# Performance work log

Hardware: AMD Instinct MI355X
Metric: run time of the kernel (lower is better)

## Reference

```python
import jax, jax.numpy as jnp
import numpy as np

EPS = 1e-12  # matches torch.nn.functional.normalize eps

def _l2norm(x, axis=-1):
    n = jnp.sqrt(jnp.sum(x * x, axis=axis, keepdims=True))
    return x / jnp.maximum(n, EPS)

def setup_inputs() -> dict:
    key = jax.random.key(0)
    k1, k2 = jax.random.split(key)
    B, C, H, W = 16, 256, 32, 32
    K = 8192
    z = jax.random.normal(k1, (B, C, H, W), dtype=jnp.float32)
    # torch init: uniform(-1/K, 1/K)
    emb_weight = jax.random.uniform(k2, (K, C), dtype=jnp.float32,
                                    minval=-1.0 / K, maxval=1.0 / K)
    return {"z": z, "emb_weight": emb_weight}

def reference(z, emb_weight):
    B, C, H, W = z.shape
    zt = jnp.transpose(z, (0, 2, 3, 1))            # [B,H,W,C]
    z_flat = zt.reshape(-1, C)                      # [N,C]
    zf_n = _l2norm(z_flat)                          # normalized tokens
    e_n = _l2norm(emb_weight)                       # normalized codebook [K,C]
    # squared euclidean distance via matmul (N x K)
    d = (jnp.sum(zf_n * zf_n, axis=1, keepdims=True)
         + jnp.sum(e_n * e_n, axis=1)
         - 2.0 * jnp.einsum('nc,kc->nk', zf_n, e_n))
    idx = jnp.argmin(d, axis=1)                     # [N]
    # get_codebook_entry: gather raw weight then normalize
    zq = _l2norm(emb_weight[idx])                   # [N,C]
    zq = zq.reshape(B, H, W, C)
    z_n = _l2norm(zt)                               # normalize z over channel dim
    # straight-through estimator
    zq = z_n + jax.lax.stop_gradient(zq - z_n)
    out = jnp.transpose(zq, (0, 3, 1, 2))           # [B,C,H,W]
    indices = idx.reshape(B, H, W)
    return out, indices
```

## Files before the change

### kernel.cpp

```cpp
#include <hip/hip_runtime.h>
#include <math.h>
#include <float.h>

#define K_CODES 8192
#define C_DIM   256
#define N_TOK   16384
#define B_      16
#define H_      32
#define W_      32
#define HW      1024
#define KSPLIT  16
#define TOKS_PER_BLK 256

typedef short  short8   __attribute__((ext_vector_type(8)));
typedef float  floatx16 __attribute__((ext_vector_type(16)));

__device__ inline ushort f32_to_bf16_rne(float x) {
    union { float f; unsigned u; } v; v.f = x;
    unsigned u = v.u;
    return (ushort)((u + 0x7FFFu + ((u >> 16) & 1u)) >> 16);
}
__device__ inline float bf16_bits_to_f32(ushort h) {
    union { unsigned u; float f; } v; v.u = ((unsigned)h) << 16;
    return v.f;
}
__device__ inline unsigned umax_(unsigned a, unsigned b) { return a > b ? a : b; }
__device__ inline unsigned umin_(unsigned a, unsigned b) { return a < b ? a : b; }

__device__ inline void g2l16(const void* g, void* l) {
    __builtin_amdgcn_global_load_lds((const __attribute__((address_space(1))) unsigned int*)g,
                                     (__attribute__((address_space(3))) unsigned int*)l,
                                     16, 0, 0);
}


__global__ __launch_bounds__(256) void norm_pack(
        const float* __restrict__ emb, const float* __restrict__ z,
        float* __restrict__ e_n, float* __restrict__ s2,
        ushort* __restrict__ Chi,
        float* __restrict__ ztn, ushort* __restrict__ Thi) {
    __shared__ float tile[32][257];
    __shared__ float pvt[32][9];
    __shared__ float pvt2[32][9];
    __shared__ float inv[32];
    int t = threadIdx.x;
    int bid = blockIdx.x;
    if (bid < 256) {
        int k0 = bid * 32;
        int r = t >> 3, cp = t & 7;
        const float* src = emb + (size_t)(k0 + r) * C_DIM + cp * 32;
        float ss = 0.f;
        #pragma unroll
        for (int j = 0; j < 8; ++j) {
            float4 v = *(const float4*)(src + j * 4);
            tile[r][cp * 32 + j * 4 + 0] = v.x;
            tile[r][cp * 32 + j * 4 + 1] = v.y;
            tile[r][cp * 32 + j * 4 + 2] = v.z;
            tile[r][cp * 32 + j * 4 + 3] = v.w;
            ss = fmaf(v.x, v.x, ss); ss = fmaf(v.y, v.y, ss);
            ss = fmaf(v.z, v.z, ss); ss = fmaf(v.w, v.w, ss);
        }
        pvt[r][cp] = ss;
        __syncthreads();
        if (t < 32) {
            float a = 0.f;
            #pragma unroll
            for (int p = 0; p < 8; ++p) a += pvt[t][p];
            inv[t] = 1.0f / fmaxf(sqrtf(a), 1e-12f);
        }
        __syncthreads();
        float iv = inv[r];
        float s2p = 0.f;
        float* dst = e_n + (size_t)(k0 + r) * C_DIM + cp * 32;
        #pragma unroll
        for (int j = 0; j < 8; ++j) {
            float a = tile[r][cp * 32 + j * 4 + 0] * iv;
            float b = tile[r][cp * 32 + j * 4 + 1] * iv;
            float c = tile[r][cp * 32 + j * 4 + 2] * iv;
            float d = tile[r][cp * 32 + j * 4 + 3] * iv;
            s2p = fmaf(a, a, s2p); s2p = fmaf(b, b, s2p);
            s2p = fmaf(c, c, s2p); s2p = fmaf(d, d, s2p);
            float4 o = {a, b, c, d};
            *(float4*)(dst + j * 4) = o;
        }
        pvt2[r][cp] = s2p;
        __syncthreads();
        if (t < 32) {
            float a = 0.f;
            #pragma unroll
            for (int p = 0; p < 8; ++p) a += pvt2[t][p];
            s2[k0 + t] = a;
        }
        char* chiB = (char*)Chi;
        #pragma unroll
        for (int e = 0; e < 4; ++e) {
            int p = e * 256 + t;
            int row = p & 31;
            int ch0 = ((p >> 6) << 4) | (((p >> 5) & 1) << 3);
            float rv = inv[row];
            union { ushort u[8]; uint4 v; } hs;
            #pragma unroll
            for (int i = 0; i < 8; ++i)
                hs.u[i] = f32_to_bf16_rne(tile[row][ch0 + i] * rv);
            size_t addr = (size_t)bid * 16384 + (size_t)p * 16;
            *(uint4*)(chiB + addr) = hs.v;
        }
    } else {
        int tb = bid - 256;
        int b = tb >> 5, h = tb & 31;
        const float* zb = z + ((size_t)(b * C_DIM) * H_ + h) * W_;
        int c0 = t >> 3, wq = t & 7;
        #pragma unroll
        for (int it = 0; it < 8; ++it) {
            int c = it * 32 + c0;
            float4 v = *(const float4*)(zb + (size_t)c * HW + wq * 4);
            tile[wq * 4 + 0][c] = v.x;
            tile[wq * 4 + 1][c] = v.y;
            tile[wq * 4 + 2][c] = v.z;
            tile[wq * 4 + 3][c] = v.w;
        }
        __syncthreads();
        int part = t >> 5, w2 = t & 31;
        float s = 0.f;
        #pragma unroll
        for (int i = 0; i < 32; ++i) {
            float v = tile[w2][part * 32 + i];
            s = fmaf(v, v, s);
        }
        pvt[w2][part] = s;
        __syncthreads();
        if (t < 32) {
            float ss = 0.f;
            #pragma unroll
            for (int p = 0; p < 8; ++p) ss += pvt[t][p];
            inv[t] = 1.0f / fmaxf(sqrtf(ss), 1e-12f);
        }
        __syncthreads();
        int n_base = tb * 32;
        for (int r = 0; r < 32; ++r) {
            float val = tile[r][t] * inv[r];
            ztn[(size_t)(n_base + r) * C_DIM + t] = val;
        }
        char* thiB = (char*)Thi;
        #pragma unroll
        for (int e = 0; e < 4; ++e) {
            int p = e * 256 + t;
            int row = p & 31;
            int ch0 = ((p >> 6) << 4) | (((p >> 5) & 1) << 3);
            float rv = inv[row];
            union { ushort u[8]; uint4 v; } hs;
            #pragma unroll
            for (int i = 0; i < 8; ++i)
                hs.u[i] = f32_to_bf16_rne(tile[row][ch0 + i] * rv);
            size_t addr = (size_t)tb * 16384 + (size_t)p * 16;
            *(uint4*)(thiB + addr) = hs.v;
        }
    }
}

__global__ __launch_bounds__(256, 2) void score_topk(
        const ushort* __restrict__ Chi,
        const ushort* __restrict__ Thi, uint2* __restrict__ cand) {
    __shared__ __align__(16) char smem[24576];
    int t = threadIdx.x;
    int l = t & 63, wv = t >> 6;
    int hh = l >> 5, col = l & 31;
    int tokBase = blockIdx.x * TOKS_PER_BLK;
    int tokRG = tokBase >> 5;
    int part = blockIdx.y;
    int partBase = part * (K_CODES / KSPLIT);
    int codeRGbase = partBase >> 5;

    const char* chiB = (const char*)Chi;
    const char* thiB = (const char*)Thi;

    unsigned rv1[2] = {0u, 0u}, rv2[2] = {0u, 0u}, rv3[2] = {0u, 0u};
    int ri1[2] = {0, 0}, ri2[2] = {0, 0}, ri3[2] = {0, 0};

    auto stage = [&](int skt, int ss, char* buf) {
        int codeRG = codeRGbase + skt * 4;
        #pragma unroll
        for (int gi = 0; gi < 3; ++gi) {
            int slice = wv * 3 + gi;
            const char* gb;
            int off;
            if (slice < 4) {
                gb = chiB + (size_t)(codeRG + slice) * 16384;
                off = slice << 10;
            } else {
                int trg = slice - 4;
                gb = thiB + (size_t)(tokRG + trg) * 16384;
                off = 4096 + (trg << 10);
            }
            g2l16(gb + ss * 1024 + (l << 4), buf + off);
        }
    };

    stage(0, 0, smem);

    for (int kt = 0; kt < 4; ++kt) {
        floatx16 acc[4][2];
        #pragma unroll
        for (int ct = 0; ct < 4; ++ct)
            #pragma unroll
            for (int nt = 0; nt < 2; ++nt)
                #pragma unroll
                for (int r = 0; r < 16; ++r) acc[ct][nt][r] = 0.f;

        for (int s = 0; s < 16; ++s) {
            int gidx = kt * 16 + s;
            __syncthreads();
            int nidx = gidx + 1;
            if (nidx < 64)
                stage(nidx >> 4, nidx & 15, smem + ((nidx & 1) ? 12288 : 0));
            const char* buf = smem + ((gidx & 1) ? 12288 : 0);

            short8 bh[2];
            #pragma unroll
            for (int nt = 0; nt < 2; ++nt) {
                int trg = wv * 2 + nt;
                bh[nt] = *(const short8*)(buf + 4096 + (trg << 10) + (l << 4));
            }
            #pragma unroll
            for (int ct = 0; ct < 4; ++ct) {
                short8 ah = *(const short8*)(buf + (ct << 10) + (l << 4));
                #pragma unroll
                for (int nt = 0; nt < 2; ++nt) {
                    acc[ct][nt] = __builtin_amdgcn_mfma_f32_32x32x16_bf16(ah, bh[nt], acc[ct][nt], 0, 0, 0);
                }
            }
        }

        int kbase = partBase + kt * 128;
        #pragma unroll
        for (int nt = 0; nt < 2; ++nt) {
            unsigned m1 = 0u, m2 = 0u, m3 = 0u;
            #pragma unroll
            for (int ct = 0; ct < 4; ++ct) {
                #pragma unroll
                for (int r = 0; r < 16; ++r) {
                    unsigned key = (__float_as_uint(fmaf(acc[ct][nt][r], 0.25f, 1.25f)) & 0xFFFFFFC0u)
                                   | (unsigned)((ct << 4) | r);
                    unsigned t1 = umin_(m1, key); m1 = umax_(m1, key);
                    unsigned t2 = umin_(m2, t1);  m2 = umax_(m2, t1);
                    m3 = umax_(m3, t2);
                }
            }
            unsigned mm[3] = {m1, m2, m3};
            #pragma unroll
            for (int j = 0; j < 3; ++j) {
                unsigned k = mm[j];
                int o = (int)(k & 63u), r = o & 15;
                int c = kbase + ((o >> 4) << 5) + (r & 3) + 8 * (r >> 2) + 4 * hh;
                if (k > rv1[nt]) {
                    rv3[nt] = rv2[nt]; ri3[nt] = ri2[nt];
                    rv2[nt] = rv1[nt]; ri2[nt] = ri1[nt];
                    rv1[nt] = k; ri1[nt] = c;
                } else if (k > rv2[nt]) {
                    rv3[nt] = rv2[nt]; ri3[nt] = ri2[nt];
                    rv2[nt] = k; ri2[nt] = c;
                } else if (k > rv3[nt]) {
                    rv3[nt] = k; ri3[nt] = c;
                }
            }
        }
    }

    __syncthreads();
    unsigned* mk = (unsigned*)smem;
    int*      mi = (int*)(smem + 8192);
    #pragma unroll
    for (int nt = 0; nt < 2; ++nt) {
        int base = (wv * 64 + nt * 32 + col) * 6 + hh * 3;
        mk[base + 0] = rv1[nt]; mi[base + 0] = ri1[nt];
        mk[base + 1] = rv2[nt]; mi[base + 1] = ri2[nt];
        mk[base + 2] = rv3[nt]; mi[base + 2] = ri3[nt];
    }
    __syncthreads();
    {
        unsigned b1 = 0u, b2 = 0u, b3 = 0u;
        int i1 = 0x7FFFFFFF, i2 = 0x7FFFFFFF, i3 = 0x7FFFFFFF;
        #pragma unroll
        for (int j = 0; j < 6; ++j) {
            unsigned k = mk[t * 6 + j]; int i = mi[t * 6 + j];
            if (k > b1 || (k == b1 && i < i1)) {
                b3 = b2; i3 = i2; b2 = b1; i2 = i1; b1 = k; i1 = i;
            } else if (k > b2 || (k == b2 && i < i2)) {
                b3 = b2; i3 = i2; b2 = k; i2 = i;
            } else if (k > b3 || (k == b3 && i < i3)) {
                b3 = k; i3 = i;
            }
        }
        size_t base = ((size_t)part * N_TOK + tokBase + t) * 3;
        cand[base + 0] = {b1, (unsigned)i1};
        cand[base + 1] = {b2, (unsigned)i2};
        cand[base + 2] = {b3, (unsigned)i3};
    }
}

__global__ __launch_bounds__(256) void rescore_gather(
        const float* __restrict__ ztn, const float* __restrict__ e_n,
        const float* __restrict__ s2, const uint2* __restrict__ cand,
        float* __restrict__ out, float* __restrict__ idxf) {
    __shared__ __align__(16) char sm[32 * 257 * 4];
    __shared__ uint2 cd[32][48];
    __shared__ int idxs[32];
    __shared__ int slowlist[32];
    __shared__ unsigned bkey[32];
    __shared__ int nslow;
    float* tile = (float*)sm;
    int t = threadIdx.x;
    int bid = blockIdx.x;
    int b = bid >> 5, h = bid & 31;
    int n_base = bid * 32;
    int wv = t >> 6, l = t & 63;

    if (t == 0) nslow = 0;
    {
        int tok = t >> 3, p = t & 7;
        int n = n_base + tok;
        #pragma unroll
        for (int slot = 0; slot < 3; ++slot) {
            cd[tok][p * 3 + slot]        = cand[((size_t)p * N_TOK + n) * 3 + slot];
            cd[tok][(p + 8) * 3 + slot]  = cand[((size_t)(p + 8) * N_TOK + n) * 3 + slot];
        }
    }
    __syncthreads();

    if (t < 32) {
        unsigned b1k = 0u, b2k = 0u; int b1i = 0x7FFFFFFF, b2i = 0x7FFFFFFF;
        #pragma unroll
        for (int p = 0; p < 48; ++p) {
            uint2 c2 = cd[t][p];
            unsigned k = c2.x; int i = (int)c2.y;
            if (k > b1k || (k == b1k && i < b1i)) { b2k = b1k; b2i = b1i; b1k = k; b1i = i; }
            else if (k > b2k || (k == b2k && i < b2i)) { b2k = k; b2i = i; }
        }
        bkey[t] = b1k;
        if (b1k - b2k > 2048u) {
            idxs[t] = b1i;
            idxf[n_base + t] = (float)b1i;
        } else {
            int s = atomicAdd(&nslow, 1);
            slowlist[s] = t;
        }
    }
    __syncthreads();
    int ns = nslow;
    for (int j = wv; j < ns; j += 4) {
        int tok = slowlist[j];
        int n = n_base + tok;
        unsigned bk = bkey[tok];
        float bs = FLT_MAX; int bi = 0x7FFFFFFF;
        if (l < 48) {
            uint2 c2 = cd[tok][l];
            if (c2.x + 8192u >= bk) {
                int c = (int)c2.y;
                const float* er = e_n + (size_t)c * C_DIM;
                const float* zr = ztn + (size_t)n * C_DIM;
                float s = 0.f;
                #pragma unroll
                for (int jj = 0; jj < 64; ++jj) {
                    float4 e4 = *(const float4*)(er + jj * 4);
                    float4 z4 = *(const float4*)(zr + jj * 4);
                    s = fmaf(e4.x, z4.x, s); s = fmaf(e4.y, z4.y, s);
                    s = fmaf(e4.z, z4.z, s); s = fmaf(e4.w, z4.w, s);
                }
                bs = s2[c] - 2.f * s;
                bi = c;
            }
        }
        #pragma unroll
        for (int d = 1; d < 64; d <<= 1) {
            float os = __shfl_xor(bs, d);
            int   oi = __shfl_xor(bi, d);
            if (os < bs || (os == bs && oi < bi)) { bs = os; bi = oi; }
        }
        if (l == 0) { idxs[tok] = bi; idxf[n] = (float)bi; }
    }
    __syncthreads();

    for (int r = 0; r < 32; ++r) {
        int k = idxs[r];
        tile[r * 257 + t] = e_n[(size_t)k * C_DIM + t];
    }
    __syncthreads();
    int w = t & 31, c0 = t >> 5;
    float* ob = out + ((size_t)(b * C_DIM) * H_ + h) * W_;
    #pragma unroll
    for (int it = 0; it < 32; ++it) {
        int c = it * 8 + c0;
        ob[(size_t)c * HW + w] = tile[w * 257 + c];
    }
}

extern "C" void kernel_launch(void* const* d_in, const int* in_sizes, int n_in,
                              void* d_out, int out_size, void* d_ws, size_t ws_size,
                              hipStream_t stream) {
    const float* z   = (const float*)d_in[0];
    const float* emb = (const float*)d_in[1];
    float* out  = (float*)d_out;
    float* idxf = out + (size_t)B_ * C_DIM * H_ * W_;

    char* ws = (char*)d_ws;
    size_t o = 0;
    float*  e_n  = (float*)(ws + o);  o += (size_t)K_CODES * C_DIM * 4;
    float*  s2   = (float*)(ws + o);  o += 32768;
    float*  ztn  = (float*)(ws + o);  o += (size_t)N_TOK * C_DIM * 4;
    ushort* Chi  = (ushort*)(ws + o); o += (size_t)K_CODES * C_DIM * 2;
    ushort* Thi  = (ushort*)(ws + o); o += (size_t)N_TOK * C_DIM * 2;
    uint2*  cand = (uint2*)(ws + o);  o += (size_t)KSPLIT * N_TOK * 3 * 8;

    hipLaunchKernelGGL(norm_pack, dim3(256 + B_ * H_), dim3(256), 0, stream,
                       emb, z, e_n, s2, Chi, ztn, Thi);
    hipLaunchKernelGGL(score_topk, dim3(N_TOK / TOKS_PER_BLK, KSPLIT), dim3(256), 0, stream,
                       Chi, Thi, cand);
    hipLaunchKernelGGL(rescore_gather, dim3(B_ * H_), dim3(256), 0, stream,
                       ztn, e_n, s2, cand, out, idxf);
}
```

Baseline: 176.5 us.

## Split score tile into 2x2 wave grid with 128-token blocks and higher occupancy

The score_topk block tile shrinks from 256 tokens to 128 tokens per block, and the four waves are arranged as a 2x2 grid over codes and tokens instead of each wave covering all codes. The kernel now uses 16KB of LDS and launch bounds allow 4 blocks per CU, aiming for better latency hiding and more blocks to spread across CUs. Staging uses precomputed global pointers advanced per step, and the final merge reduces 12 candidates per token instead of 6. In exchange each block reuses less data, since the codebook slice is streamed once per 128 tokens rather than per 256, which doubles codebook traffic.

Measured after the change: 208.4 us. 18.0% more time.

```diff
diff --git a/kernel.cpp b/kernel.cpp
--- a/kernel.cpp
+++ b/kernel.cpp
@@ -10,7 +10,7 @@
 #define W_      32
 #define HW      1024
 #define KSPLIT  16
-#define TOKS_PER_BLK 256
+#define TOKS_PER_BLK 128
 
 typedef short  short8   __attribute__((ext_vector_type(8)));
 typedef float  floatx16 __attribute__((ext_vector_type(16)));
@@ -158,13 +158,14 @@
     }
 }
 
-__global__ __launch_bounds__(256, 2) void score_topk(
+__global__ __launch_bounds__(256, 4) void score_topk(
         const ushort* __restrict__ Chi,
         const ushort* __restrict__ Thi, uint2* __restrict__ cand) {
-    __shared__ __align__(16) char smem[24576];
+    __shared__ __align__(16) char smem[16384];
     int t = threadIdx.x;
     int l = t & 63, wv = t >> 6;
     int hh = l >> 5, col = l & 31;
+    int wr = wv >> 1, wc = wv & 1;
     int tokBase = blockIdx.x * TOKS_PER_BLK;
     int tokRG = tokBase >> 5;
     int part = blockIdx.y;
@@ -174,61 +175,62 @@
     const char* chiB = (const char*)Chi;
     const char* thiB = (const char*)Thi;
 
+    const char* gp[2];
+    int ldo[2];
+    int dkt[2];
+    #pragma unroll
+    for (int gi = 0; gi < 2; ++gi) {
+        int sl = wv * 2 + gi;
+        if (sl < 4) {
+            gp[gi]  = chiB + (size_t)(codeRGbase + sl) * 16384 + (l << 4);
+            ldo[gi] = sl << 10;
+            dkt[gi] = 4 * 16384 - 15 * 1024;
+        } else {
+            int trg = sl - 4;
+            gp[gi]  = thiB + (size_t)(tokRG + trg) * 16384 + (l << 4);
+            ldo[gi] = 4096 + (trg << 10);
+            dkt[gi] = -15 * 1024;
+        }
+    }
+    auto issue = [&](int parity) {
+        char* base = smem + (parity ? 8192 : 0);
+        g2l16(gp[0], base + ldo[0]);
+        g2l16(gp[1], base + ldo[1]);
+    };
+    auto advance = [&](int snum) {
+        bool kb = (snum & 15) == 15;
+        gp[0] += kb ? dkt[0] : 1024;
+        gp[1] += kb ? dkt[1] : 1024;
+    };
+
+    issue(0); advance(0);
+
     unsigned rv1[2] = {0u, 0u}, rv2[2] = {0u, 0u}, rv3[2] = {0u, 0u};
     int ri1[2] = {0, 0}, ri2[2] = {0, 0}, ri3[2] = {0, 0};
 
-    auto stage = [&](int skt, int ss, char* buf) {
-        int codeRG = codeRGbase + skt * 4;
-        #pragma unroll
-        for (int gi = 0; gi < 3; ++gi) {
-            int slice = wv * 3 + gi;
-            const char* gb;
-            int off;
-            if (slice < 4) {
-                gb = chiB + (size_t)(codeRG + slice) * 16384;
-                off = slice << 10;
-            } else {
-                int trg = slice - 4;
-                gb = thiB + (size_t)(tokRG + trg) * 16384;
-                off = 4096 + (trg << 10);
-            }
-            g2l16(gb + ss * 1024 + (l << 4), buf + off);
-        }
-    };
-
-    stage(0, 0, smem);
-
     for (int kt = 0; kt < 4; ++kt) {
-        floatx16 acc[4][2];
-        #pragma unroll
-        for (int ct = 0; ct < 4; ++ct)
+        floatx16 acc[2][2];
+        #pragma unroll
+        for (int ct = 0; ct < 2; ++ct)
             #pragma unroll
             for (int nt = 0; nt < 2; ++nt)
                 #pragma unroll
                 for (int r = 0; r < 16; ++r) acc[ct][nt][r] = 0.f;
 
-        for (int s = 0; s < 16; ++s) {
-            int gidx = kt * 16 + s;
+        for (int ss = 0; ss < 16; ++ss) {
+            int g = kt * 16 + ss;
             __syncthreads();
-            int nidx = gidx + 1;
-            if (nidx < 64)
-                stage(nidx >> 4, nidx & 15, smem + ((nidx & 1) ? 12288 : 0));
-            const char* buf = smem + ((gidx & 1) ? 12288 : 0);
-
-            short8 bh[2];
-            #pragma unroll
-            for (int nt = 0; nt < 2; ++nt) {
-                int trg = wv * 2 + nt;
-                bh[nt] = *(const short8*)(buf + 4096 + (trg << 10) + (l << 4));
-            }
-            #pragma unroll
-            for (int ct = 0; ct < 4; ++ct) {
-                short8 ah = *(const short8*)(buf + (ct << 10) + (l << 4));
-                #pragma unroll
-                for (int nt = 0; nt < 2; ++nt) {
-                    acc[ct][nt] = __builtin_amdgcn_mfma_f32_32x32x16_bf16(ah, bh[nt], acc[ct][nt], 0, 0, 0);
-                }
-            }
+            if (g + 1 < 64) { issue((g + 1) & 1); advance(g + 1); }
+            const char* buf = smem + ((g & 1) ? 8192 : 0);
+
+            short8 ah0 = *(const short8*)(buf + (((wc << 1) | 0) << 10) + (l << 4));
+            short8 ah1 = *(const short8*)(buf + (((wc << 1) | 1) << 10) + (l << 4));
+            short8 bh0 = *(const short8*)(buf + 4096 + (((wr << 1) | 0) << 10) + (l << 4));
+            short8 bh1 = *(const short8*)(buf + 4096 + (((wr << 1) | 1) << 10) + (l << 4));
+            acc[0][0] = __builtin_amdgcn_mfma_f32_32x32x16_bf16(ah0, bh0, acc[0][0], 0, 0, 0);
+            acc[0][1] = __builtin_amdgcn_mfma_f32_32x32x16_bf16(ah0, bh1, acc[0][1], 0, 0, 0);
+            acc[1][0] = __builtin_amdgcn_mfma_f32_32x32x16_bf16(ah1, bh0, acc[1][0], 0, 0, 0);
+            acc[1][1] = __builtin_amdgcn_mfma_f32_32x32x16_bf16(ah1, bh1, acc[1][1], 0, 0, 0);
         }
 
         int kbase = partBase + kt * 128;
@@ -236,11 +238,11 @@
         for (int nt = 0; nt < 2; ++nt) {
             unsigned m1 = 0u, m2 = 0u, m3 = 0u;
             #pragma unroll
-            for (int ct = 0; ct < 4; ++ct) {
+            for (int ct = 0; ct < 2; ++ct) {
                 #pragma unroll
                 for (int r = 0; r < 16; ++r) {
                     unsigned key = (__float_as_uint(fmaf(acc[ct][nt][r], 0.25f, 1.25f)) & 0xFFFFFFC0u)
-                                   | (unsigned)((ct << 4) | r);
+                                   | (unsigned)(((((wc << 1) | ct)) << 4) | r);
                     unsigned t1 = umin_(m1, key); m1 = umax_(m1, key);
                     unsigned t2 = umin_(m2, t1);  m2 = umax_(m2, t1);
                     m3 = umax_(m3, t2);
@@ -271,18 +273,18 @@
     int*      mi = (int*)(smem + 8192);
     #pragma unroll
     for (int nt = 0; nt < 2; ++nt) {
-        int base = (wv * 64 + nt * 32 + col) * 6 + hh * 3;
+        int base = (wr * 64 + nt * 32 + col) * 12 + (((wc << 1) | hh)) * 3;
         mk[base + 0] = rv1[nt]; mi[base + 0] = ri1[nt];
         mk[base + 1] = rv2[nt]; mi[base + 1] = ri2[nt];
         mk[base + 2] = rv3[nt]; mi[base + 2] = ri3[nt];
     }
     __syncthreads();
-    {
+    if (t < 128) {
         unsigned b1 = 0u, b2 = 0u, b3 = 0u;
         int i1 = 0x7FFFFFFF, i2 = 0x7FFFFFFF, i3 = 0x7FFFFFFF;
         #pragma unroll
-        for (int j = 0; j < 6; ++j) {
-            unsigned k = mk[t * 6 + j]; int i = mi[t * 6 + j];
+        for (int j = 0; j < 12; ++j) {
+            unsigned k = mk[t * 12 + j]; int i = mi[t * 12 + j];
             if (k > b1 || (k == b1 && i < i1)) {
                 b3 = b2; i3 = i2; b2 = b1; i2 = i1; b1 = k; i1 = i;
             } else if (k > b2 || (k == b2 && i < i2)) {
```

## Split rescore and gather into separate decide_rescore and gather_out kernels

Applied to the files above, without the earlier changes.

Splits the combined rescore-and-gather kernel into two kernels. The first processes 256 tokens per block with one thread per token: it merges the candidates, writes the index directly, and rescores ambiguous tokens with one wavefront each, reading candidates straight from global memory. The second reads the indices back and does the transposed gather into the output. This is meant to parallelise the candidate merge across all threads, which previously ran on only 32 threads per block, and to balance the slow-path work. The cost is an extra launch and a round trip of the indices through memory.

Result: slower. 203.4 us (+15.2%).

```diff
diff --git a/kernel.cpp b/kernel.cpp
--- a/kernel.cpp
+++ b/kernel.cpp
@@ -19,10 +19,6 @@
     union { float f; unsigned u; } v; v.f = x;
     unsigned u = v.u;
     return (ushort)((u + 0x7FFFu + ((u >> 16) & 1u)) >> 16);
-}
-__device__ inline float bf16_bits_to_f32(ushort h) {
-    union { unsigned u; float f; } v; v.u = ((unsigned)h) << 16;
-    return v.f;
 }
 __device__ inline unsigned umax_(unsigned a, unsigned b) { return a > b ? a : b; }
 __device__ inline unsigned umin_(unsigned a, unsigned b) { return a < b ? a : b; }
@@ -298,90 +294,83 @@
     }
 }
 
-__global__ __launch_bounds__(256) void rescore_gather(
+__global__ __launch_bounds__(256) void decide_rescore(
         const float* __restrict__ ztn, const float* __restrict__ e_n,
         const float* __restrict__ s2, const uint2* __restrict__ cand,
-        float* __restrict__ out, float* __restrict__ idxf) {
-    __shared__ __align__(16) char sm[32 * 257 * 4];
-    __shared__ uint2 cd[32][48];
-    __shared__ int idxs[32];
-    __shared__ int slowlist[32];
-    __shared__ unsigned bkey[32];
+        float* __restrict__ idxf) {
+    __shared__ int slowlist[256];
+    __shared__ unsigned slowbk[256];
     __shared__ int nslow;
-    float* tile = (float*)sm;
+    int t = threadIdx.x;
+    int n0 = blockIdx.x * 256;
+    int wv = t >> 6, l = t & 63;
+    if (t == 0) nslow = 0;
+    __syncthreads();
+    {
+        int n = n0 + t;
+        unsigned b1k = 0u, b2k = 0u; int b1i = 0x7FFFFFFF, b2i = 0x7FFFFFFF;
+        for (int p = 0; p < 16; ++p) {
+            #pragma unroll
+            for (int s = 0; s < 3; ++s) {
+                uint2 c2 = cand[((size_t)p * N_TOK + n) * 3 + s];
+                unsigned k = c2.x; int i = (int)c2.y;
+                if (k > b1k || (k == b1k && i < b1i)) { b2k = b1k; b2i = b1i; b1k = k; b1i = i; }
+                else if (k > b2k || (k == b2k && i < b2i)) { b2k = k; b2i = i; }
+            }
+        }
+        if (b1k - b2k > 2048u) {
+            idxf[n] = (float)b1i;
+        } else {
+            int s = atomicAdd(&nslow, 1);
+            slowlist[s] = t; slowbk[s] = b1k;
+        }
+    }
+    __syncthreads();
+    int ns = nslow;
+    for (int j = wv; j < ns; j += 4) {
+        int tok = slowlist[j];
+        int n = n0 + tok;
+        unsigned bk = slowbk[j];
+        float bs = FLT_MAX; int bi = 0x7FFFFFFF;
+        if (l < 48) {
+            int p = l / 3, s = l - p * 3;
+            uint2 c2 = cand[((size_t)p * N_TOK + n) * 3 + s];
+            if (c2.x + 8192u >= bk) {
+                int c = (int)c2.y;
+                const float* er = e_n + (size_t)c * C_DIM;
+                const float* zr = ztn + (size_t)n * C_DIM;
+                float sdot = 0.f;
+                #pragma unroll
+                for (int jj = 0; jj < 64; ++jj) {
+                    float4 e4 = *(const float4*)(er + jj * 4);
+                    float4 z4 = *(const float4*)(zr + jj * 4);
+                    sdot = fmaf(e4.x, z4.x, sdot); sdot = fmaf(e4.y, z4.y, sdot);
+                    sdot = fmaf(e4.z, z4.z, sdot); sdot = fmaf(e4.w, z4.w, sdot);
+                }
+                bs = s2[c] - 2.f * sdot;
+                bi = c;
+            }
+        }
+        #pragma unroll
+        for (int d = 1; d < 64; d <<= 1) {
+            float os = __shfl_xor(bs, d);
+            int   oi = __shfl_xor(bi, d);
+            if (os < bs || (os == bs && oi < bi)) { bs = os; bi = oi; }
+        }
+        if (l == 0) idxf[n] = (float)bi;
+    }
+}
+
+__global__ __launch_bounds__(256) void gather_out(
+        const float* __restrict__ e_n, const float* __restrict__ idxf,
+        float* __restrict__ out) {
+    __shared__ float tile[32 * 257];
     int t = threadIdx.x;
     int bid = blockIdx.x;
     int b = bid >> 5, h = bid & 31;
     int n_base = bid * 32;
-    int wv = t >> 6, l = t & 63;
-
-    if (t == 0) nslow = 0;
-    {
-        int tok = t >> 3, p = t & 7;
-        int n = n_base + tok;
-        #pragma unroll
-        for (int slot = 0; slot < 3; ++slot) {
-            cd[tok][p * 3 + slot]        = cand[((size_t)p * N_TOK + n) * 3 + slot];
-            cd[tok][(p + 8) * 3 + slot]  = cand[((size_t)(p + 8) * N_TOK + n) * 3 + slot];
-        }
-    }
-    __syncthreads();
-
-    if (t < 32) {
-        unsigned b1k = 0u, b2k = 0u; int b1i = 0x7FFFFFFF, b2i = 0x7FFFFFFF;
-        #pragma unroll
-        for (int p = 0; p < 48; ++p) {
-            uint2 c2 = cd[t][p];
-            unsigned k = c2.x; int i = (int)c2.y;
-            if (k > b1k || (k == b1k && i < b1i)) { b2k = b1k; b2i = b1i; b1k = k; b1i = i; }
-            else if (k > b2k || (k == b2k && i < b2i)) { b2k = k; b2i = i; }
-        }
-        bkey[t] = b1k;
-        if (b1k - b2k > 2048u) {
-            idxs[t] = b1i;
-            idxf[n_base + t] = (float)b1i;
-        } else {
-            int s = atomicAdd(&nslow, 1);
-            slowlist[s] = t;
-        }
-    }
-    __syncthreads();
-    int ns = nslow;
-    for (int j = wv; j < ns; j += 4) {
-        int tok = slowlist[j];
-        int n = n_base + tok;
-        unsigned bk = bkey[tok];
-        float bs = FLT_MAX; int bi = 0x7FFFFFFF;
-        if (l < 48) {
-            uint2 c2 = cd[tok][l];
-            if (c2.x + 8192u >= bk) {
-                int c = (int)c2.y;
-                const float* er = e_n + (size_t)c * C_DIM;
-                const float* zr = ztn + (size_t)n * C_DIM;
-                float s = 0.f;
-                #pragma unroll
-                for (int jj = 0; jj < 64; ++jj) {
-                    float4 e4 = *(const float4*)(er + jj * 4);
-                    float4 z4 = *(const float4*)(zr + jj * 4);
-                    s = fmaf(e4.x, z4.x, s); s = fmaf(e4.y, z4.y, s);
-                    s = fmaf(e4.z, z4.z, s); s = fmaf(e4.w, z4.w, s);
-                }
-                bs = s2[c] - 2.f * s;
-                bi = c;
-            }
-        }
-        #pragma unroll
-        for (int d = 1; d < 64; d <<= 1) {
-            float os = __shfl_xor(bs, d);
-            int   oi = __shfl_xor(bi, d);
-            if (os < bs || (os == bs && oi < bi)) { bs = os; bi = oi; }
-        }
-        if (l == 0) { idxs[tok] = bi; idxf[n] = (float)bi; }
-    }
-    __syncthreads();
-
     for (int r = 0; r < 32; ++r) {
-        int k = idxs[r];
+        int k = (int)idxf[n_base + r];
         tile[r * 257 + t] = e_n[(size_t)k * C_DIM + t];
     }
     __syncthreads();
@@ -415,6 +404,8 @@
                        emb, z, e_n, s2, Chi, ztn, Thi);
     hipLaunchKernelGGL(score_topk, dim3(N_TOK / TOKS_PER_BLK, KSPLIT), dim3(256), 0, stream,
                        Chi, Thi, cand);
-    hipLaunchKernelGGL(rescore_gather, dim3(B_ * H_), dim3(256), 0, stream,
-                       ztn, e_n, s2, cand, out, idxf);
-}
+    hipLaunchKernelGGL(decide_rescore, dim3(N_TOK / 256), dim3(256), 0, stream,
+                       ztn, e_n, s2, cand, idxf);
+    hipLaunchKernelGGL(gather_out, dim3(B_ * H_), dim3(256), 0, stream,
+                       e_n, idxf, out);
+}
```
